# Performance work log

Measured on AMD Instinct MI355X. Metric: run time of the kernel, lower is better.

## Reference

```python
import jax, jax.numpy as jnp
import numpy as np

COUNT_BINS = 8
BOUND = 3.0
MIN_BIN_WIDTH = 1e-3
MIN_BIN_HEIGHT = 1e-3
MIN_DERIVATIVE = 1e-3
EPS = 1e-6


def _made_masks(D, H1, H2, M):
    indeg = np.arange(1, D + 1)                     # input degrees 1..D
    h1 = np.arange(H1) % (D - 1) + 1                # hidden degrees in [1, D-1]
    h2 = np.arange(H2) % (D - 1) + 1
    outdeg = np.tile(indeg, M)                      # (M*D,), reshape-compatible with (M, D)
    m1 = (h1[:, None] >= indeg[None, :]).astype(np.float32)   # (H1, D)
    m2 = (h2[:, None] >= h1[None, :]).astype(np.float32)      # (H2, H1)
    m3 = (outdeg[:, None] > h2[None, :]).astype(np.float32)   # (M*D, H2)
    return jnp.asarray(m1), jnp.asarray(m2), jnp.asarray(m3)


def _rq_spline_forward(x, w, h, d):
    # x: (B, D); w, h: (B, D, K) simplex weights; d: (B, D, K-1) softplus'd interior derivatives
    K = w.shape[-1]
    left, right = -BOUND, BOUND

    widths = MIN_BIN_WIDTH + (1.0 - MIN_BIN_WIDTH * K) * w
    heights = MIN_BIN_HEIGHT + (1.0 - MIN_BIN_HEIGHT * K) * h
    derivs = MIN_DERIVATIVE + d
    ones = jnp.ones_like(derivs[..., :1])
    derivs = jnp.concatenate([ones, derivs, ones], -1)          # (B, D, K+1), boundary slope 1

    cw = jnp.cumsum(widths, -1)
    edge_l = jnp.full_like(cw[..., :1], left)
    edge_r = jnp.full_like(cw[..., :1], right)
    cumw = jnp.concatenate([edge_l, left + (right - left) * cw[..., :-1], edge_r], -1)  # (B, D, K+1)
    widths = cumw[..., 1:] - cumw[..., :-1]
    ch = jnp.cumsum(heights, -1)
    cumh = jnp.concatenate([edge_l, left + (right - left) * ch[..., :-1], edge_r], -1)
    heights = cumh[..., 1:] - cumh[..., :-1]

    inside = (x >= left) & (x <= right)
    xc = jnp.clip(x, left, right)
    # pyro: bin_idx = sum(x >= cumwidths + eps) - 1
    idx = jnp.sum((xc[..., None] >= (cumw + EPS)).astype(jnp.int32), -1) - 1
    idx = jnp.clip(idx, 0, K - 1)                               # (B, D)

    def g(t):
        return jnp.take_along_axis(t, idx[..., None], axis=-1)[..., 0]

    x_k, w_k = g(cumw), g(widths)
    y_k, h_k = g(cumh), g(heights)
    delta = h_k / w_k
    d_k, d_k1 = g(derivs), g(derivs[..., 1:])

    theta = (xc - x_k) / w_k
    tt = theta * (1.0 - theta)
    num = h_k * (delta * theta ** 2 + d_k * tt)
    den = delta + (d_k + d_k1 - 2.0 * delta) * tt
    y = y_k + num / den
    dnum = delta ** 2 * (d_k1 * theta ** 2 + 2.0 * delta * tt + d_k * (1.0 - theta) ** 2)
    ld = jnp.log(dnum) - 2.0 * jnp.log(den)
    return jnp.where(inside, y, x), jnp.where(inside, ld, jnp.zeros_like(ld))


def _forward(x, W1, b1, W2, b2, W3, b3):
    B, D = x.shape
    H1, H2 = W1.shape[0], W2.shape[0]
    K = COUNT_BINS
    M = 3 * K - 1
    m1, m2, m3 = _made_masks(D, H1, H2, M)
    h1 = jax.nn.relu(x @ (W1 * m1).T + b1)
    h2 = jax.nn.relu(h1 @ (W2 * m2).T + b2)
    p = (h2 @ (W3 * m3).T + b3).reshape(B, M, D)                # (B, 3K-1, D)
    w = jax.nn.softmax(jnp.swapaxes(p[:, :K, :], 1, 2), axis=-1)          # (B, D, K)
    hgt = jax.nn.softmax(jnp.swapaxes(p[:, K:2 * K, :], 1, 2), axis=-1)   # (B, D, K)
    d = jax.nn.softplus(jnp.swapaxes(p[:, 2 * K:, :], 1, 2))              # (B, D, K-1)
    z, ld = _rq_spline_forward(x, w, hgt, d)
    return z, ld.sum(-1)


def setup_inputs() -> dict:
    key = jax.random.key(0)
    ks = jax.random.split(key, 7)
    B, D, H1, H2 = 32768, 64, 64, 32
    M = 3 * COUNT_BINS - 1
    s1, s2, s3 = 1.0 / np.sqrt(D), 1.0 / np.sqrt(H1), 1.0 / np.sqrt(H2)
    return {
        "x": jax.random.normal(ks[0], (B, D), jnp.float32),
        "W1": jax.random.uniform(ks[1], (H1, D), jnp.float32, -s1, s1),
        "b1": jax.random.uniform(ks[2], (H1,), jnp.float32, -s1, s1),
        "W2": jax.random.uniform(ks[3], (H2, H1), jnp.float32, -s2, s2),
        "b2": jax.random.uniform(ks[4], (H2,), jnp.float32, -s2, s2),
        "W3": jax.random.uniform(ks[5], (M * D, H2), jnp.float32, -s3, s3),
        "b3": jax.random.uniform(ks[6], (M * D,), jnp.float32, -s3, s3),
    }


def reference(x, W1, b1, W2, b2, W3, b3):
    return _forward(x, W1, b1, W2, b2, W3, b3)
```

## Files before the change

### kernel.cpp

```cpp
#include <hip/hip_runtime.h>

#define NM 23

typedef short short8 __attribute__((ext_vector_type(8)));
typedef float f32x4 __attribute__((ext_vector_type(4)));

#define LOG2E 1.44269504088896340736f

__device__ __forceinline__ float softplus_f(float v) {
  return fmaxf(v, 0.f) + __logf(1.f + __expf(-fabsf(v)));
}

__device__ __forceinline__ float fastrcp(float v) {
  return __builtin_amdgcn_rcpf(v);
}

__device__ __forceinline__ unsigned short bf16_rne(float x) {
  unsigned u = __float_as_uint(x);
  u += 0x7FFFu + ((u >> 16) & 1u);
  return (unsigned short)(u >> 16);
}

__global__ __launch_bounds__(256) void prep_kernel(
    const float* __restrict__ W1, const float* __restrict__ W2,
    const float* __restrict__ W3,
    unsigned short* __restrict__ B1hi,
    unsigned short* __restrict__ B2hi,
    unsigned short* __restrict__ B3hi) {
  const int idx = blockIdx.x * 256 + threadIdx.x;
  const int j = idx & 7, lane = (idx >> 3) & 63;
  const int col = lane & 15, quad = lane >> 4;

  if (idx < 4096) {
    const int rest = idx >> 9, kt = rest & 1, nt = rest >> 1;
    const int k = kt * 32 + quad * 8 + j;
    const int n = nt * 16 + col;
    const float v = ((n % 63) >= k) ? W1[n * 64 + k] : 0.f;
    B1hi[idx] = bf16_rne(v);
  }
  if (idx < 2048) {
    const int rest = idx >> 9, kt = rest & 1, nt = rest >> 1;
    const int k = kt * 32 + quad * 8 + j;
    const int n = nt * 16 + col;
    const float v = ((k % 63) <= n) ? W2[n * 64 + k] : 0.f;
    B2hi[idx] = bf16_rne(v);
  }
  if (idx < 92 * 64 * 8) {
    const int nt = idx >> 9;
    const int n = nt * 16 + col;
    const int d = n & 63;
    const int m = n >> 6;
    const int k = quad * 8 + j;
    float v = (k < d) ? W3[(size_t)n * 32 + k] : 0.f;
    if (m < 16) v *= LOG2E;
    B3hi[idx] = bf16_rne(v);
  }
}

__device__ __forceinline__ short8 cvt_hi(const float* src) {
  const f32x4 a0 = *reinterpret_cast<const f32x4*>(src);
  const f32x4 a1 = *reinterpret_cast<const f32x4*>(src + 4);
  const float af[8] = {a0.x, a0.y, a0.z, a0.w, a1.x, a1.y, a1.z, a1.w};
  short8 hi;
  #pragma unroll
  for (int j = 0; j < 8; ++j) hi[j] = (short)bf16_rne(af[j]);
  return hi;
}

__global__ __launch_bounds__(256, 4) void fused_kernel(
    const float* __restrict__ x,
    const unsigned short* __restrict__ B1hi,
    const float* __restrict__ b1,
    const unsigned short* __restrict__ B2hi,
    const float* __restrict__ b2,
    const unsigned short* __restrict__ B3hi,
    const float* __restrict__ b3,
    float* __restrict__ out, int B) {
  __shared__ float h1s[16][68];
  __shared__ float h2s[16][68];
  __shared__ float b3s[64 * NM];
  __shared__ float ldp[4][16];

  const int t = threadIdx.x;
  const int b0 = blockIdx.x * 16;

  for (int idx = t; idx < 64 * NM; idx += 256) {
    const int dl = idx / NM, m = idx - dl * NM;
    const float s = (m < 16) ? LOG2E : 1.f;
    b3s[idx] = b3[m * 64 + dl] * s;
  }
  __syncthreads();

  const int lane = t & 63;
  const int wv   = __builtin_amdgcn_readfirstlane(t >> 6);
  const int col  = lane & 15;
  const int quad = lane >> 4;

  {
    const int nt1 = wv;
    const float* xrow = x + (size_t)(b0 + col) * 64;
    short8 ah[2];
    #pragma unroll
    for (int kt = 0; kt < 2; ++kt)
      ah[kt] = cvt_hi(xrow + kt * 32 + quad * 8);

    const float bv = b1[nt1 * 16 + col];
    f32x4 acc = {bv, bv, bv, bv};
    #pragma unroll
    for (int kt = 0; kt < 2; ++kt) {
      const size_t off = ((size_t)(nt1 * 2 + kt) * 64 + lane) * 8;
      const short8 bh = *reinterpret_cast<const short8*>(B1hi + off);
      acc = __builtin_amdgcn_mfma_f32_16x16x32_bf16(ah[kt], bh, acc, 0, 0, 0);
    }
    #pragma unroll
    for (int reg = 0; reg < 4; ++reg)
      h1s[quad * 4 + reg][nt1 * 16 + col] = fmaxf(acc[reg], 0.f);
  }
  __syncthreads();

  if (wv < 2) {
    const int nt2 = wv;
    short8 ah[2];
    #pragma unroll
    for (int kt = 0; kt < 2; ++kt)
      ah[kt] = cvt_hi(&h1s[col][kt * 32 + quad * 8]);

    const float bv = b2[nt2 * 16 + col];
    f32x4 acc = {bv, bv, bv, bv};
    #pragma unroll
    for (int kt = 0; kt < 2; ++kt) {
      const size_t off = ((size_t)(nt2 * 2 + kt) * 64 + lane) * 8;
      const short8 bh = *reinterpret_cast<const short8*>(B2hi + off);
      acc = __builtin_amdgcn_mfma_f32_16x16x32_bf16(ah[kt], bh, acc, 0, 0, 0);
    }
    #pragma unroll
    for (int reg = 0; reg < 4; ++reg)
      h2s[quad * 4 + reg][nt2 * 16 + col] = fmaxf(acc[reg], 0.f);
  }
  __syncthreads();

  const int dc = wv;
  const int row0 = quad * 4;
  const int d = dc * 16 + col;

  const short8 ah = cvt_hi(&h2s[col][quad * 8]);

  float xvv[4];
  #pragma unroll
  for (int reg = 0; reg < 4; ++reg)
    xvv[reg] = x[(size_t)(b0 + row0 + reg) * 64 + d];

  __syncthreads();

  float ldr[4] = {0.f, 0.f, 0.f, 0.f};
  const float WSC = 1.0f - 1e-3f * 8.0f;

  float xcv[4], fidx[4], xkv[4], wkv[4], ykv[4], hkv[4];

  {
    f32x4 accW[8], accH[8];
    #pragma unroll
    for (int m = 0; m < 8; ++m) {
      const float bw = b3s[d * NM + m];
      const float bh2 = b3s[d * NM + (8 + m)];
      accW[m] = (f32x4){bw, bw, bw, bw};
      accH[m] = (f32x4){bh2, bh2, bh2, bh2};
    }
    #pragma unroll
    for (int m = 0; m < 8; ++m) {
      const size_t offW = ((size_t)(4 * m + dc) * 64 + lane) * 8;
      const size_t offH = ((size_t)(4 * (8 + m) + dc) * 64 + lane) * 8;
      const short8 bW = *reinterpret_cast<const short8*>(B3hi + offW);
      const short8 bH = *reinterpret_cast<const short8*>(B3hi + offH);
      accW[m] = __builtin_amdgcn_mfma_f32_16x16x32_bf16(ah, bW, accW[m], 0, 0, 0);
      accH[m] = __builtin_amdgcn_mfma_f32_16x16x32_bf16(ah, bH, accH[m], 0, 0, 0);
    }
    #pragma unroll
    for (int reg = 0; reg < 4; ++reg) {
      float ew[8], eh[8], sw = 0.f, sh = 0.f;
      #pragma unroll
      for (int k = 0; k < 8; ++k) {
        ew[k] = exp2f(accW[k][reg]); sw += ew[k];
        eh[k] = exp2f(accH[k][reg]); sh += eh[k];
      }
      const float scaleW = 6.f * WSC * fastrcp(sw);
      const float scaleH = 6.f * WSC * fastrcp(sh);
      float cumw[9], cumh[9];
      cumw[0] = -3.f; cumh[0] = -3.f;
      float prefW = 0.f, prefH = 0.f;
      #pragma unroll
      for (int k = 0; k < 7; ++k) {
        const float Ck = -3.f + 6e-3f * (float)(k + 1);
        prefW += ew[k];
        prefH += eh[k];
        cumw[k + 1] = fmaf(prefW, scaleW, Ck);
        cumh[k + 1] = fmaf(prefH, scaleH, Ck);
      }
      cumw[8] = 3.f; cumh[8] = 3.f;

      const float xv = xvv[reg];
      const float xc = fminf(fmaxf(xv, -3.f), 3.f);
      float fi = 0.f, xk = cumw[0], xk1 = cumw[1];
      #pragma unroll
      for (int k = 1; k < 8; ++k) {
        const bool s = xc >= cumw[k] + 1e-6f;
        xk  = s ? cumw[k]     : xk;
        xk1 = s ? cumw[k + 1] : xk1;
        fi  = s ? (float)k    : fi;
      }
      float yk = cumh[0], yk1 = cumh[1];
      #pragma unroll
      for (int k = 1; k < 8; ++k) {
        const bool s = fi >= (float)k;
        yk  = s ? cumh[k]     : yk;
        yk1 = s ? cumh[k + 1] : yk1;
      }
      xcv[reg] = xc; fidx[reg] = fi; xkv[reg] = xk; wkv[reg] = xk1 - xk;
      ykv[reg] = yk; hkv[reg] = yk1 - yk;
    }
  }

  {
    f32x4 acc[7];
    #pragma unroll
    for (int m = 0; m < 7; ++m) {
      const float bv = b3s[d * NM + (16 + m)];
      acc[m] = (f32x4){bv, bv, bv, bv};
    }
    #pragma unroll
    for (int m = 0; m < 7; ++m) {
      const size_t off = ((size_t)(4 * (16 + m) + dc) * 64 + lane) * 8;
      const short8 bh = *reinterpret_cast<const short8*>(B3hi + off);
      acc[m] = __builtin_amdgcn_mfma_f32_16x16x32_bf16(ah, bh, acc[m], 0, 0, 0);
    }
    #pragma unroll
    for (int reg = 0; reg < 4; ++reg) {
      float p[7];
      #pragma unroll
      for (int k = 0; k < 7; ++k) p[k] = acc[k][reg];
      const float fi = fidx[reg];

      float pa = p[0], pb = p[0];
      #pragma unroll
      for (int k = 2; k < 8; ++k) pa = (fi >= (float)k) ? p[k - 1] : pa;
      #pragma unroll
      for (int k = 1; k < 7; ++k) pb = (fi >= (float)k) ? p[k] : pb;
      const float spa = 1e-3f + softplus_f(pa);
      const float spb = 1e-3f + softplus_f(pb);
      const float dk  = (fi >= 0.5f) ? spa : 1.f;
      const float dk1 = (fi >= 6.5f) ? 1.f : spb;

      const float xc = xcv[reg], xk = xkv[reg], wk = wkv[reg];
      const float yk = ykv[reg], hk = hkv[reg];
      const float invwk = fastrcp(wk);
      const float delta = hk * invwk;
      const float theta = (xc - xk) * invwk;
      const float omt = 1.f - theta;
      const float tt = theta * omt;
      const float th2 = theta * theta;
      const float num = hk * (delta * th2 + dk * tt);
      const float den = delta + (dk + dk1 - 2.f * delta) * tt;
      const float rden = fastrcp(den);
      const float yv = yk + num * rden;
      const float dnum =
          delta * delta * (dk1 * th2 + 2.f * delta * tt + dk * omt * omt);
      const float ldv = __logf(dnum * rden * rden);

      const float xv = xvv[reg];
      const bool inside = (xv >= -3.f) && (xv <= 3.f);
      h2s[row0 + reg][d] = inside ? yv : xv;
      ldr[reg] += inside ? ldv : 0.f;
    }
  }

  #pragma unroll
  for (int mask = 1; mask <= 8; mask <<= 1) {
    #pragma unroll
    for (int reg = 0; reg < 4; ++reg)
      ldr[reg] += __shfl_xor(ldr[reg], mask, 64);
  }
  if (col == 0) {
    #pragma unroll
    for (int reg = 0; reg < 4; ++reg)
      ldp[dc][row0 + reg] = ldr[reg];
  }

  __syncthreads();

  if (t < 16)
    out[(size_t)B * 64 + b0 + t] =
        (ldp[0][t] + ldp[1][t]) + (ldp[2][t] + ldp[3][t]);

  {
    const int rr = t >> 4, c4 = (t & 15) * 4;
    const float4 v = make_float4(h2s[rr][c4 + 0], h2s[rr][c4 + 1],
                                 h2s[rr][c4 + 2], h2s[rr][c4 + 3]);
    *reinterpret_cast<float4*>(out + (size_t)(b0 + rr) * 64 + c4) = v;
  }
}

extern "C" void kernel_launch(void* const* d_in, const int* in_sizes, int n_in,
                              void* d_out, int out_size, void* d_ws, size_t ws_size,
                              hipStream_t stream) {
  const float* x  = (const float*)d_in[0];
  const float* W1 = (const float*)d_in[1];
  const float* b1 = (const float*)d_in[2];
  const float* W2 = (const float*)d_in[3];
  const float* b2 = (const float*)d_in[4];
  const float* W3 = (const float*)d_in[5];
  const float* b3 = (const float*)d_in[6];
  float* out = (float*)d_out;
  char* ws   = (char*)d_ws;

  unsigned short* B1hi = (unsigned short*)(ws);
  unsigned short* B2hi = (unsigned short*)(ws + 8192);
  unsigned short* B3hi = (unsigned short*)(ws + 16384);

  const int B = in_sizes[0] / 64;

  prep_kernel<<<184, 256, 0, stream>>>(W1, W2, W3, B1hi, B2hi, B3hi);

  fused_kernel<<<B / 16, 256, 0, stream>>>(
      x, B1hi, b1, B2hi, b2, B3hi, b3, out, B);
}
```

Baseline: 103.1 us.

## Make bias staging and epilogue per-wave, dropping block barriers

Each wave now stages only its own 16 columns of the layer-3 bias into a per-wave shared slice, so no block-wide barrier is needed before the MLP. The x loads are hoisted to the start of the kernel to hide their latency. The spline results go to the free h1s buffer, and each wave stores its own 16-column slab of the output. The log-det cross-wave reduction becomes global atomicAdds, which removes two more __syncthreads. The atomics only give the right sum if the log-det output starts at zero, and no zeroing is added here.

```diff
diff --git a/kernel.cpp b/kernel.cpp
--- a/kernel.cpp
+++ b/kernel.cpp
@@ -78,23 +78,29 @@
     float* __restrict__ out, int B) {
   __shared__ float h1s[16][68];
   __shared__ float h2s[16][68];
-  __shared__ float b3s[64 * NM];
-  __shared__ float ldp[4][16];
+  __shared__ float b3w[4][NM][16];
 
   const int t = threadIdx.x;
   const int b0 = blockIdx.x * 16;
-
-  for (int idx = t; idx < 64 * NM; idx += 256) {
-    const int dl = idx / NM, m = idx - dl * NM;
-    const float s = (m < 16) ? LOG2E : 1.f;
-    b3s[idx] = b3[m * 64 + dl] * s;
-  }
-  __syncthreads();
 
   const int lane = t & 63;
   const int wv   = __builtin_amdgcn_readfirstlane(t >> 6);
   const int col  = lane & 15;
   const int quad = lane >> 4;
+  const int dc   = wv;
+  const int row0 = quad * 4;
+  const int d    = dc * 16 + col;
+
+  for (int idx = lane; idx < NM * 16; idx += 64) {
+    const int m = idx >> 4, c = idx & 15;
+    const float s = (m < 16) ? LOG2E : 1.f;
+    b3w[wv][m][c] = b3[m * 64 + dc * 16 + c] * s;
+  }
+
+  float xvv[4];
+  #pragma unroll
+  for (int reg = 0; reg < 4; ++reg)
+    xvv[reg] = x[(size_t)(b0 + row0 + reg) * 64 + d];
 
   {
     const int nt1 = wv;
@@ -139,18 +145,7 @@
   }
   __syncthreads();
 
-  const int dc = wv;
-  const int row0 = quad * 4;
-  const int d = dc * 16 + col;
-
   const short8 ah = cvt_hi(&h2s[col][quad * 8]);
-
-  float xvv[4];
-  #pragma unroll
-  for (int reg = 0; reg < 4; ++reg)
-    xvv[reg] = x[(size_t)(b0 + row0 + reg) * 64 + d];
-
-  __syncthreads();
 
   float ldr[4] = {0.f, 0.f, 0.f, 0.f};
   const float WSC = 1.0f - 1e-3f * 8.0f;
@@ -161,8 +156,8 @@
     f32x4 accW[8], accH[8];
     #pragma unroll
     for (int m = 0; m < 8; ++m) {
-      const float bw = b3s[d * NM + m];
-      const float bh2 = b3s[d * NM + (8 + m)];
+      const float bw = b3w[wv][m][col];
+      const float bh2 = b3w[wv][8 + m][col];
       accW[m] = (f32x4){bw, bw, bw, bw};
       accH[m] = (f32x4){bh2, bh2, bh2, bh2};
     }
@@ -224,7 +219,7 @@
     f32x4 acc[7];
     #pragma unroll
     for (int m = 0; m < 7; ++m) {
-      const float bv = b3s[d * NM + (16 + m)];
+      const float bv = b3w[wv][16 + m][col];
       acc[m] = (f32x4){bv, bv, bv, bv};
     }
     #pragma unroll
@@ -268,7 +263,7 @@
 
       const float xv = xvv[reg];
       const bool inside = (xv >= -3.f) && (xv <= 3.f);
-      h2s[row0 + reg][d] = inside ? yv : xv;
+      h1s[row0 + reg][d] = inside ? yv : xv;
       ldr[reg] += inside ? ldv : 0.f;
     }
   }
@@ -282,20 +277,17 @@
   if (col == 0) {
     #pragma unroll
     for (int reg = 0; reg < 4; ++reg)
-      ldp[dc][row0 + reg] = ldr[reg];
-  }
-
-  __syncthreads();
-
-  if (t < 16)
-    out[(size_t)B * 64 + b0 + t] =
-        (ldp[0][t] + ldp[1][t]) + (ldp[2][t] + ldp[3][t]);
+      atomicAdd(out + (size_t)B * 64 + b0 + row0 + reg, ldr[reg]);
+  }
 
   {
-    const int rr = t >> 4, c4 = (t & 15) * 4;
-    const float4 v = make_float4(h2s[rr][c4 + 0], h2s[rr][c4 + 1],
-                                 h2s[rr][c4 + 2], h2s[rr][c4 + 3]);
-    *reinterpret_cast<float4*>(out + (size_t)(b0 + rr) * 64 + c4) = v;
+    const int rr = lane >> 2, ci = (lane & 3) * 4;
+    const float4 v = make_float4(h1s[rr][dc * 16 + ci + 0],
+                                 h1s[rr][dc * 16 + ci + 1],
+                                 h1s[rr][dc * 16 + ci + 2],
+                                 h1s[rr][dc * 16 + ci + 3]);
+    *reinterpret_cast<float4*>(
+        out + (size_t)(b0 + rr) * 64 + dc * 16 + ci) = v;
   }
 }
 
```

New measurement: 96.93 us. 1.06x faster.
